# Kernel optimization log

Hardware: AMD Instinct MI355X
Metric: run time of the kernel (lower is better)

The kernel has to match this reference:

```python
import math
import jax, jax.numpy as jnp
import numpy as np

HIDDEN = 1024

def setup_inputs() -> dict:
    key = jax.random.key(0)
    kx, kq, kk, kv = jax.random.split(key, 4)
    scale = 1.0 / math.sqrt(HIDDEN)
    x = jax.random.normal(kx, (4, 2048, HIDDEN), dtype=jnp.float32)
    # nn.Linear weights, stored as [out, in] like torch; y = x @ W.T
    Wq = jax.random.normal(kq, (HIDDEN, HIDDEN), dtype=jnp.float32) * scale
    Wk = jax.random.normal(kk, (HIDDEN, HIDDEN), dtype=jnp.float32) * scale
    Wv = jax.random.normal(kv, (HIDDEN, HIDDEN), dtype=jnp.float32) * scale
    return {"x": x, "Wq": Wq, "Wk": Wk, "Wv": Wv}

def reference(x, Wq, Wk, Wv):
    # Q,K,V: [b, s, d]
    Q = jnp.einsum('bsd,ed->bse', x, Wq)
    K = jnp.einsum('bsd,ed->bse', x, Wk)
    V = jnp.einsum('bsd,ed->bse', x, Wv)
    scores = jnp.einsum('bqd,bkd->bqk', Q, K) / math.sqrt(x.shape[-1])
    att = jax.nn.softmax(scores, axis=-1)  # stable max-subtracted softmax, same math as _softmax
    return jnp.einsum('bqk,bkd->bqd', att, V)
```

## Files before the change

kernel.cpp:

```cpp
#include <hip/hip_runtime.h>
#include <stdint.h>

typedef unsigned int uint;
typedef unsigned short ushort;
typedef __attribute__((ext_vector_type(8))) short short8;
typedef __attribute__((ext_vector_type(16))) float floatx16;

#define MEG (1024u * 1024u)

__device__ inline ushort f2b(float f) {
  union { float f; uint u; } c; c.f = f;
  uint u = c.u;
  u = (u + 0x7fffu + ((u >> 16) & 1u)) >> 16;
  return (ushort)u;
}
__device__ inline float b2f(ushort u) {
  union { uint i; float f; } c; c.i = ((uint)u) << 16; return c.f;
}

__device__ inline void gl_lds16(const ushort* g, ushort* l) {
  __builtin_amdgcn_global_load_lds(
      (const __attribute__((address_space(1))) void*)g,
      (__attribute__((address_space(3))) void*)l, 16, 0, 0);
}

__global__ __launch_bounds__(256) void cvt_all(
    const float* __restrict__ x,  const float* __restrict__ wq,
    const float* __restrict__ wk, const float* __restrict__ wv,
    ushort* __restrict__ xb, ushort* __restrict__ wb)
{
  const int b = blockIdx.x;
  const float* s; ushort* d; int i;
  if (b < 4096) {
    s = x; d = xb; i = b * 256 + threadIdx.x;
  } else {
    int t = b - 4096;
    int wsel = t >> 9;
    s = (wsel == 0) ? wq : (wsel == 1) ? wk : wv;
    d = wb + (size_t)wsel * MEG;
    i = (t & 511) * 256 + threadIdx.x;
  }
  float4 a = ((const float4*)s)[i * 2];
  float4 c = ((const float4*)s)[i * 2 + 1];
  short8 v;
  v[0] = (short)f2b(a.x); v[1] = (short)f2b(a.y);
  v[2] = (short)f2b(a.z); v[3] = (short)f2b(a.w);
  v[4] = (short)f2b(c.x); v[5] = (short)f2b(c.y);
  v[6] = (short)f2b(c.z); v[7] = (short)f2b(c.w);
  ((short8*)d)[i] = v;
}

template <int MODE, int BN>
__device__ __forceinline__ void gemm_core(
    const ushort* __restrict__ A, int lda, size_t sA,
    const ushort* __restrict__ B, int ldb, size_t sB,
    void* __restrict__ C, int ldc, size_t sC,
    int K, float scale, float* __restrict__ Lsum)
{
  constexpr int NJ = BN / 64;
  constexpr int NB = BN / 32;
  __shared__ ushort As[128 * 64];
  __shared__ ushort Bs[BN * 64];
  __shared__ float Linv[(MODE == 2) ? 128 : 1];

  const int tid = threadIdx.x;
  const int bz  = blockIdx.z;
  A += (size_t)bz * sA;
  B += (size_t)bz * sB;

  const int m0 = blockIdx.y * 128;
  const int n0 = blockIdx.x * BN;

  const int lane = tid & 63;
  const int w    = tid >> 6;
  const int l32  = lane & 31;
  const int lh   = lane >> 5;
  const int mw   = w >> 1;
  const int nw   = w & 1;

  if constexpr (MODE == 2) {
    if (tid < 128) {
      float s = 0.f;
#pragma unroll
      for (int p = 0; p < 32; ++p)
        s += Lsum[((size_t)p * gridDim.z + bz) * 2048 + m0 + tid];
      Linv[tid] = 1.0f / s;
    }
  }

  const int srow = tid >> 3;
  const ushort* agp[4];
  const ushort* bgp[NB];
#pragma unroll
  for (int c4 = 0; c4 < 4; ++c4) {
    int r   = c4 * 32 + srow;
    int col = (((tid & 7) ^ ((r ^ (r >> 3)) & 7))) * 8;
    agp[c4] = A + (size_t)(m0 + r) * lda + col;
  }
#pragma unroll
  for (int cb = 0; cb < NB; ++cb) {
    int r   = cb * 32 + srow;
    int col = (((tid & 7) ^ ((r ^ (r >> 3)) & 7))) * 8;
    bgp[cb] = B + (size_t)(n0 + r) * ldb + col;
  }

  int arow[2], aswz[2], brow[NJ], bswz[NJ];
#pragma unroll
  for (int t = 0; t < 2; ++t) {
    arow[t] = mw * 64 + t * 32 + l32;
    aswz[t] = (arow[t] ^ (arow[t] >> 3)) & 7;
  }
#pragma unroll
  for (int t = 0; t < NJ; ++t) {
    brow[t] = nw * (BN / 2) + t * 32 + l32;
    bswz[t] = (brow[t] ^ (brow[t] >> 3)) & 7;
  }

  floatx16 acc[2][NJ];
#pragma unroll
  for (int i = 0; i < 2; ++i)
#pragma unroll
    for (int j = 0; j < NJ; ++j)
#pragma unroll
      for (int r = 0; r < 16; ++r) acc[i][j][r] = 0.f;

  for (int k0 = 0; k0 < K; k0 += 64) {
    __syncthreads();
#pragma unroll
    for (int c4 = 0; c4 < 4; ++c4) {
      gl_lds16(agp[c4], &As[(c4 * 32 + w * 8) * 64]);
      agp[c4] += 64;
    }
#pragma unroll
    for (int cb = 0; cb < NB; ++cb) {
      gl_lds16(bgp[cb], &Bs[(cb * 32 + w * 8) * 64]);
      bgp[cb] += 64;
    }
    __syncthreads();

#pragma unroll
    for (int s = 0; s < 4; ++s) {
      short8 af[2], bf[NJ];
#pragma unroll
      for (int t = 0; t < 2; ++t)
        af[t] = *(const short8*)&As[arow[t] * 64 + (((s * 2 + lh) ^ aswz[t]) * 8)];
#pragma unroll
      for (int t = 0; t < NJ; ++t)
        bf[t] = *(const short8*)&Bs[brow[t] * 64 + (((s * 2 + lh) ^ bswz[t]) * 8)];
#pragma unroll
      for (int i = 0; i < 2; ++i)
#pragma unroll
        for (int j = 0; j < NJ; ++j)
          acc[i][j] = __builtin_amdgcn_mfma_f32_32x32x16_bf16(
              af[i], bf[j], acc[i][j], 0, 0, 0);
    }
  }

  if constexpr (MODE == 0) {
#pragma unroll
    for (int i = 0; i < 2; ++i)
#pragma unroll
      for (int j = 0; j < NJ; ++j) {
        const int mbase = m0 + mw * 64 + i * 32 + 4 * lh;
        const int ng    = n0 + nw * (BN / 2) + j * 32 + l32;
        if (ng < 2048) {
          ushort* dst = (ushort*)C + (size_t)(ng >> 10) * (8u * MEG);
          const int nn = ng & 1023;
#pragma unroll
          for (int g = 0; g < 4; ++g)
#pragma unroll
            for (int r = 0; r < 4; ++r)
              dst[(size_t)(mbase + 8 * g + r) * 1024 + nn] =
                  f2b(acc[i][j][4 * g + r]);
        } else {
          ushort* Vo = (ushort*)C + (size_t)16 * MEG;
#pragma unroll
          for (int g = 0; g < 4; ++g) {
            uint lo = (uint)f2b(acc[i][j][4 * g + 0]) |
                      ((uint)f2b(acc[i][j][4 * g + 1]) << 16);
            uint hi = (uint)f2b(acc[i][j][4 * g + 2]) |
                      ((uint)f2b(acc[i][j][4 * g + 3]) << 16);
            *(uint2*)&Vo[(size_t)(ng - 2048) * 8192 + mbase + 8 * g] =
                make_uint2(lo, hi);
          }
        }
      }
  } else if constexpr (MODE == 1) {
    ushort* Cb = (ushort*)C + (size_t)bz * sC;
    float* Lp = Lsum + ((size_t)(blockIdx.x * 2 + nw) * gridDim.z + bz) * 2048;
    const int ng0 = n0 + nw * (BN / 2) + l32;
#pragma unroll
    for (int i = 0; i < 2; ++i) {
      const int mbase = m0 + mw * 64 + i * 32 + 4 * lh;
#pragma unroll
      for (int g = 0; g < 4; ++g)
#pragma unroll
        for (int r = 0; r < 4; ++r) {
          const int mg = mbase + 8 * g + r;
          float p0 = exp2f(acc[i][0][4 * g + r] * scale);
          float p1 = exp2f(acc[i][NJ - 1][4 * g + r] * scale);
          ushort u0 = f2b(p0), u1 = f2b(p1);
          Cb[(size_t)mg * ldc + ng0]      = u0;
          Cb[(size_t)mg * ldc + ng0 + 32] = u1;
          float ps = b2f(u0) + b2f(u1);
#pragma unroll
          for (int d = 1; d < 32; d <<= 1) ps += __shfl_xor(ps, d);
          if (l32 == 0) Lp[mg] = ps;
        }
    }
  } else {
    float* Cb = (float*)C + (size_t)bz * sC;
#pragma unroll
    for (int i = 0; i < 2; ++i) {
      const int mbase = m0 + mw * 64 + i * 32 + 4 * lh;
#pragma unroll
      for (int g = 0; g < 4; ++g)
#pragma unroll
        for (int r = 0; r < 4; ++r) {
          const int mg = mbase + 8 * g + r;
          const float inv = Linv[mg - m0];
#pragma unroll
          for (int j = 0; j < NJ; ++j) {
            const int ng = n0 + nw * (BN / 2) + j * 32 + l32;
            Cb[(size_t)mg * ldc + ng] = acc[i][j][4 * g + r] * inv;
          }
        }
    }
  }
}

__global__ __launch_bounds__(256, 4) void gemm_qkv(
    const ushort* __restrict__ A, int lda, size_t sA,
    const ushort* __restrict__ B, int ldb, size_t sB,
    void* __restrict__ C, int ldc, size_t sC, int K, float scale,
    float* __restrict__ Lsum) {
  gemm_core<0, 128>(A, lda, sA, B, ldb, sB, C, ldc, sC, K, scale, Lsum);
}
__global__ __launch_bounds__(256, 4) void gemm_s(
    const ushort* __restrict__ A, int lda, size_t sA,
    const ushort* __restrict__ B, int ldb, size_t sB,
    void* __restrict__ C, int ldc, size_t sC, int K, float scale,
    float* __restrict__ Lsum) {
  gemm_core<1, 128>(A, lda, sA, B, ldb, sB, C, ldc, sC, K, scale, Lsum);
}
__global__ __launch_bounds__(256, 4) void gemm_pv(
    const ushort* __restrict__ A, int lda, size_t sA,
    const ushort* __restrict__ B, int ldb, size_t sB,
    void* __restrict__ C, int ldc, size_t sC, int K, float scale,
    float* __restrict__ Lsum) {
  gemm_core<2, 128>(A, lda, sA, B, ldb, sB, C, ldc, sC, K, scale, Lsum);
}

extern "C" void kernel_launch(void* const* d_in, const int* in_sizes, int n_in,
                              void* d_out, int out_size, void* d_ws, size_t ws_size,
                              hipStream_t stream) {
  const float* x  = (const float*)d_in[0];
  const float* Wq = (const float*)d_in[1];
  const float* Wk = (const float*)d_in[2];
  const float* Wv = (const float*)d_in[3];
  float* outp = (float*)d_out;

  const float SCALE = 1.4426950408889634f / 32.0f;

  ushort* W0 = (ushort*)d_ws;
  ushort* Qb = W0;
  ushort* Kb = W0 + (size_t)8 * MEG;
  ushort* Vt = W0 + (size_t)16 * MEG;
  ushort* xb = W0 + (size_t)24 * MEG;
  ushort* Wb = W0 + (size_t)32 * MEG;
  ushort* Pb = W0 + (size_t)24 * MEG;

  const size_t NEED_FULL = ((size_t)40 * MEG) * 2 + (size_t)32 * 4 * 2048 * 4;
  const bool full = ws_size >= NEED_FULL;
  float* Lp = full ? (float*)(W0 + (size_t)40 * MEG)
                   : (float*)(W0 + (size_t)28 * MEG);

  cvt_all<<<5632, 256, 0, stream>>>(x, Wq, Wk, Wv, xb, Wb);

  gemm_qkv<<<dim3(24, 64, 1), 256, 0, stream>>>(
      xb, 1024, 0, Wb, 1024, 0, Qb, 1024, 0, 1024, 1.f, nullptr);

  if (full) {
    gemm_s<<<dim3(16, 16, 4), 256, 0, stream>>>(
        Qb, 1024, (size_t)2048 * 1024, Kb, 1024, (size_t)2048 * 1024,
        Pb, 2048, (size_t)2048 * 2048, 1024, SCALE, Lp);
    gemm_pv<<<dim3(8, 16, 4), 256, 0, stream>>>(
        Pb, 2048, (size_t)2048 * 2048, Vt, 8192, 2048,
        outp, 1024, (size_t)2048 * 1024, 2048, 1.f, Lp);
  } else {
    for (int b = 0; b < 4; ++b) {
      gemm_s<<<dim3(16, 16, 1), 256, 0, stream>>>(
          Qb + (size_t)b * 2048 * 1024, 1024, 0,
          Kb + (size_t)b * 2048 * 1024, 1024, 0,
          Pb, 2048, 0, 1024, SCALE, Lp);
      gemm_pv<<<dim3(8, 16, 1), 256, 0, stream>>>(
          Pb, 2048, 0, Vt + (size_t)b * 2048, 8192, 0,
          outp + (size_t)b * 2048 * 1024, 1024, 0, 2048, 1.f, Lp);
    }
  }
}
```

Measured before the change: 245.7 us.

## Double-buffer LDS tiles with K=32 stages to overlap loads and MFMA

Replaces the single-buffered K=64 LDS tile loop with a two-slot double buffer over K=32 slices. The next slice is issued with global_load_lds before the current slice's MFMAs run, and the swizzle changes to match the 32-wide rows. The aim is to hide global-load latency behind compute and remove one barrier per iteration. In exchange there are twice as many iterations, each with less MFMA work to hide latency behind, and a narrower swizzle that may bring LDS bank conflicts.

```diff
diff --git a/kernel.cpp b/kernel.cpp
--- a/kernel.cpp
+++ b/kernel.cpp
@@ -58,9 +58,11 @@
     int K, float scale, float* __restrict__ Lsum)
 {
   constexpr int NJ = BN / 64;
-  constexpr int NB = BN / 32;
-  __shared__ ushort As[128 * 64];
-  __shared__ ushort Bs[BN * 64];
+  constexpr int BI = BN / 64;
+  constexpr int ASLOT = 128 * 32;
+  constexpr int BSLOT = BN * 32;
+  __shared__ ushort As[2 * ASLOT];
+  __shared__ ushort Bs[2 * BSLOT];
   __shared__ float Linv[(MODE == 2) ? 128 : 1];
 
   const int tid = threadIdx.x;
@@ -88,32 +90,31 @@
     }
   }
 
-  const int srow = tid >> 3;
-  const ushort* agp[4];
-  const ushort* bgp[NB];
-#pragma unroll
-  for (int c4 = 0; c4 < 4; ++c4) {
-    int r   = c4 * 32 + srow;
-    int col = (((tid & 7) ^ ((r ^ (r >> 3)) & 7))) * 8;
-    agp[c4] = A + (size_t)(m0 + r) * lda + col;
-  }
-#pragma unroll
-  for (int cb = 0; cb < NB; ++cb) {
-    int r   = cb * 32 + srow;
-    int col = (((tid & 7) ^ ((r ^ (r >> 3)) & 7))) * 8;
-    bgp[cb] = B + (size_t)(n0 + r) * ldb + col;
+  const int srow = tid >> 2;
+  const int sch  = tid & 3;
+  const ushort* agp[2];
+  const ushort* bgp[BI];
+#pragma unroll
+  for (int q = 0; q < 2; ++q) {
+    int r = q * 64 + srow;
+    agp[q] = A + (size_t)(m0 + r) * lda + ((sch ^ ((r >> 1) & 3)) * 8);
+  }
+#pragma unroll
+  for (int q = 0; q < BI; ++q) {
+    int r = q * 64 + srow;
+    bgp[q] = B + (size_t)(n0 + r) * ldb + ((sch ^ ((r >> 1) & 3)) * 8);
   }
 
   int arow[2], aswz[2], brow[NJ], bswz[NJ];
 #pragma unroll
   for (int t = 0; t < 2; ++t) {
     arow[t] = mw * 64 + t * 32 + l32;
-    aswz[t] = (arow[t] ^ (arow[t] >> 3)) & 7;
+    aswz[t] = (arow[t] >> 1) & 3;
   }
 #pragma unroll
   for (int t = 0; t < NJ; ++t) {
     brow[t] = nw * (BN / 2) + t * 32 + l32;
-    bswz[t] = (brow[t] ^ (brow[t] >> 3)) & 7;
+    bswz[t] = (brow[t] >> 1) & 3;
   }
 
   floatx16 acc[2][NJ];
@@ -124,29 +125,38 @@
 #pragma unroll
       for (int r = 0; r < 16; ++r) acc[i][j][r] = 0.f;
 
-  for (int k0 = 0; k0 < K; k0 += 64) {
-    __syncthreads();
-#pragma unroll
-    for (int c4 = 0; c4 < 4; ++c4) {
-      gl_lds16(agp[c4], &As[(c4 * 32 + w * 8) * 64]);
-      agp[c4] += 64;
-    }
-#pragma unroll
-    for (int cb = 0; cb < NB; ++cb) {
-      gl_lds16(bgp[cb], &Bs[(cb * 32 + w * 8) * 64]);
-      bgp[cb] += 64;
-    }
-    __syncthreads();
-
-#pragma unroll
-    for (int s = 0; s < 4; ++s) {
+  const int nt = K / 32;
+
+#define STAGE(slot)                                                       \
+  {                                                                       \
+    ushort* Ad = &As[(slot) * ASLOT];                                     \
+    ushort* Bd = &Bs[(slot) * BSLOT];                                     \
+    _Pragma("unroll")                                                     \
+    for (int q = 0; q < 2; ++q) {                                         \
+      gl_lds16(agp[q], Ad + (q * 64 + w * 16) * 32); agp[q] += 32;        \
+    }                                                                     \
+    _Pragma("unroll")                                                     \
+    for (int q = 0; q < BI; ++q) {                                        \
+      gl_lds16(bgp[q], Bd + (q * 64 + w * 16) * 32); bgp[q] += 32;        \
+    }                                                                     \
+  }
+
+  STAGE(0);
+  __syncthreads();
+
+  for (int t = 0; t < nt; ++t) {
+    const ushort* At = &As[(t & 1) * ASLOT];
+    const ushort* Bt = &Bs[(t & 1) * BSLOT];
+    if (t + 1 < nt) STAGE((t + 1) & 1);
+#pragma unroll
+    for (int s = 0; s < 2; ++s) {
       short8 af[2], bf[NJ];
 #pragma unroll
-      for (int t = 0; t < 2; ++t)
-        af[t] = *(const short8*)&As[arow[t] * 64 + (((s * 2 + lh) ^ aswz[t]) * 8)];
-#pragma unroll
-      for (int t = 0; t < NJ; ++t)
-        bf[t] = *(const short8*)&Bs[brow[t] * 64 + (((s * 2 + lh) ^ bswz[t]) * 8)];
+      for (int i = 0; i < 2; ++i)
+        af[i] = *(const short8*)&At[arow[i] * 32 + (((s * 2 + lh) ^ aswz[i]) * 8)];
+#pragma unroll
+      for (int j = 0; j < NJ; ++j)
+        bf[j] = *(const short8*)&Bt[brow[j] * 32 + (((s * 2 + lh) ^ bswz[j]) * 8)];
 #pragma unroll
       for (int i = 0; i < 2; ++i)
 #pragma unroll
@@ -154,7 +164,9 @@
           acc[i][j] = __builtin_amdgcn_mfma_f32_32x32x16_bf16(
               af[i], bf[j], acc[i][j], 0, 0, 0);
     }
-  }
+    __syncthreads();
+  }
+#undef STAGE
 
   if constexpr (MODE == 0) {
 #pragma unroll
```

After: 268.8 us. 1.09x slower.

## Give PV GEMM a dedicated double-buffered LDS pipeline kernel

Applied to the files above, without the earlier changes.

Splits the P·V GEMM out of the shared templated core into its own kernel. The new kernel double-buffers the A and B tiles in LDS, issuing the global-to-LDS loads for the next K tile while MFMAs run on the current one, with one barrier per iteration. The aim is to hide global load latency in the long-K (2048) PV product. It doubles LDS usage, so launch bounds drop to 2 blocks per SM, which may lower occupancy.

```diff
diff --git a/kernel.cpp b/kernel.cpp
--- a/kernel.cpp
+++ b/kernel.cpp
@@ -61,7 +61,6 @@
   constexpr int NB = BN / 32;
   __shared__ ushort As[128 * 64];
   __shared__ ushort Bs[BN * 64];
-  __shared__ float Linv[(MODE == 2) ? 128 : 1];
 
   const int tid = threadIdx.x;
   const int bz  = blockIdx.z;
@@ -77,16 +76,6 @@
   const int lh   = lane >> 5;
   const int mw   = w >> 1;
   const int nw   = w & 1;
-
-  if constexpr (MODE == 2) {
-    if (tid < 128) {
-      float s = 0.f;
-#pragma unroll
-      for (int p = 0; p < 32; ++p)
-        s += Lsum[((size_t)p * gridDim.z + bz) * 2048 + m0 + tid];
-      Linv[tid] = 1.0f / s;
-    }
-  }
 
   const int srow = tid >> 3;
   const ushort* agp[4];
@@ -185,7 +174,7 @@
           }
         }
       }
-  } else if constexpr (MODE == 1) {
+  } else {
     ushort* Cb = (ushort*)C + (size_t)bz * sC;
     float* Lp = Lsum + ((size_t)(blockIdx.x * 2 + nw) * gridDim.z + bz) * 2048;
     const int ng0 = n0 + nw * (BN / 2) + l32;
@@ -208,24 +197,6 @@
           if (l32 == 0) Lp[mg] = ps;
         }
     }
-  } else {
-    float* Cb = (float*)C + (size_t)bz * sC;
-#pragma unroll
-    for (int i = 0; i < 2; ++i) {
-      const int mbase = m0 + mw * 64 + i * 32 + 4 * lh;
-#pragma unroll
-      for (int g = 0; g < 4; ++g)
-#pragma unroll
-        for (int r = 0; r < 4; ++r) {
-          const int mg = mbase + 8 * g + r;
-          const float inv = Linv[mg - m0];
-#pragma unroll
-          for (int j = 0; j < NJ; ++j) {
-            const int ng = n0 + nw * (BN / 2) + j * 32 + l32;
-            Cb[(size_t)mg * ldc + ng] = acc[i][j][4 * g + r] * inv;
-          }
-        }
-    }
   }
 }
 
@@ -243,12 +214,127 @@
     float* __restrict__ Lsum) {
   gemm_core<1, 128>(A, lda, sA, B, ldb, sB, C, ldc, sC, K, scale, Lsum);
 }
-__global__ __launch_bounds__(256, 4) void gemm_pv(
+
+__global__ __launch_bounds__(256, 2) void gemm_pv(
     const ushort* __restrict__ A, int lda, size_t sA,
     const ushort* __restrict__ B, int ldb, size_t sB,
     void* __restrict__ C, int ldc, size_t sC, int K, float scale,
-    float* __restrict__ Lsum) {
-  gemm_core<2, 128>(A, lda, sA, B, ldb, sB, C, ldc, sC, K, scale, Lsum);
+    float* __restrict__ Lsum)
+{
+  constexpr int SLOT = 128 * 64;
+  __shared__ ushort As[2 * SLOT];
+  __shared__ ushort Bs[2 * SLOT];
+  __shared__ float Linv[128];
+
+  const int tid = threadIdx.x;
+  const int bz  = blockIdx.z;
+  A += (size_t)bz * sA;
+  B += (size_t)bz * sB;
+
+  const int m0 = blockIdx.y * 128;
+  const int n0 = blockIdx.x * 128;
+
+  const int lane = tid & 63;
+  const int w    = tid >> 6;
+  const int l32  = lane & 31;
+  const int lh   = lane >> 5;
+  const int mw   = w >> 1;
+  const int nw   = w & 1;
+
+  if (tid < 128) {
+    float s = 0.f;
+#pragma unroll
+    for (int p = 0; p < 32; ++p)
+      s += Lsum[((size_t)p * gridDim.z + bz) * 2048 + m0 + tid];
+    Linv[tid] = 1.0f / s;
+  }
+
+  const int srow = tid >> 3;
+  const ushort* agp[4];
+  const ushort* bgp[4];
+#pragma unroll
+  for (int c4 = 0; c4 < 4; ++c4) {
+    int r   = c4 * 32 + srow;
+    int col = (((tid & 7) ^ ((r ^ (r >> 3)) & 7))) * 8;
+    agp[c4] = A + (size_t)(m0 + r) * lda + col;
+    bgp[c4] = B + (size_t)(n0 + r) * ldb + col;
+  }
+
+  int arow[2], aswz[2], brow[2], bswz[2];
+#pragma unroll
+  for (int t = 0; t < 2; ++t) {
+    arow[t] = mw * 64 + t * 32 + l32;
+    aswz[t] = (arow[t] ^ (arow[t] >> 3)) & 7;
+    brow[t] = nw * 64 + t * 32 + l32;
+    bswz[t] = (brow[t] ^ (brow[t] >> 3)) & 7;
+  }
+
+  floatx16 acc[2][2];
+#pragma unroll
+  for (int i = 0; i < 2; ++i)
+#pragma unroll
+    for (int j = 0; j < 2; ++j)
+#pragma unroll
+      for (int r = 0; r < 16; ++r) acc[i][j][r] = 0.f;
+
+  const int nt = K / 64;
+
+#define PV_STAGE(slot)                                                    \
+  {                                                                       \
+    ushort* Ad = &As[(slot) * SLOT];                                      \
+    ushort* Bd = &Bs[(slot) * SLOT];                                      \
+    _Pragma("unroll")                                                     \
+    for (int c4 = 0; c4 < 4; ++c4) {                                      \
+      gl_lds16(agp[c4], Ad + (c4 * 32 + w * 8) * 64); agp[c4] += 64;      \
+      gl_lds16(bgp[c4], Bd + (c4 * 32 + w * 8) * 64); bgp[c4] += 64;      \
+    }                                                                     \
+  }
+
+  PV_STAGE(0);
+  __syncthreads();
+
+  for (int t = 0; t < nt; ++t) {
+    const ushort* At = &As[(t & 1) * SLOT];
+    const ushort* Bt = &Bs[(t & 1) * SLOT];
+    if (t + 1 < nt) PV_STAGE((t + 1) & 1);
+
+#pragma unroll
+    for (int s = 0; s < 4; ++s) {
+      short8 af[2], bf[2];
+#pragma unroll
+      for (int i = 0; i < 2; ++i)
+        af[i] = *(const short8*)&At[arow[i] * 64 + (((s * 2 + lh) ^ aswz[i]) * 8)];
+#pragma unroll
+      for (int j = 0; j < 2; ++j)
+        bf[j] = *(const short8*)&Bt[brow[j] * 64 + (((s * 2 + lh) ^ bswz[j]) * 8)];
+#pragma unroll
+      for (int i = 0; i < 2; ++i)
+#pragma unroll
+        for (int j = 0; j < 2; ++j)
+          acc[i][j] = __builtin_amdgcn_mfma_f32_32x32x16_bf16(
+              af[i], bf[j], acc[i][j], 0, 0, 0);
+    }
+    __syncthreads();
+  }
+#undef PV_STAGE
+
+  float* Cb = (float*)C + (size_t)bz * sC;
+#pragma unroll
+  for (int i = 0; i < 2; ++i) {
+    const int mbase = m0 + mw * 64 + i * 32 + 4 * lh;
+#pragma unroll
+    for (int g = 0; g < 4; ++g)
+#pragma unroll
+      for (int r = 0; r < 4; ++r) {
+        const int mg = mbase + 8 * g + r;
+        const float inv = Linv[mg - m0];
+#pragma unroll
+        for (int j = 0; j < 2; ++j) {
+          const int ng = n0 + nw * 64 + j * 32 + l32;
+          Cb[(size_t)mg * ldc + ng] = acc[i][j][4 * g + r] * inv;
+        }
+      }
+  }
 }
 
 extern "C" void kernel_launch(void* const* d_in, const int* in_sizes, int n_in,
```

Result: slower. 252.8 us (+2.9%).

## Split-K the PV GEMM in two and normalize in a separate combine kernel

Applied to the files above, without the earlier changes.

The P·V GEMM is split along its reduction dimension into two halves, which doubles the grid so more blocks run per CU. One half writes its partial sums to the output buffer and the other to a scratch buffer placed over the no-longer-needed Q/K workspace. A new elementwise combine kernel adds the two partials, recomputes the softmax row sums from the stored partial sums, and applies the 1/sum normalization. The in-GEMM normalization is removed. In exchange, an extra launch and roughly three full fp32 output-sized memory passes are added.

```diff
diff --git a/kernel.cpp b/kernel.cpp
--- a/kernel.cpp
+++ b/kernel.cpp
@@ -61,12 +61,17 @@
   constexpr int NB = BN / 32;
   __shared__ ushort As[128 * 64];
   __shared__ ushort Bs[BN * 64];
-  __shared__ float Linv[(MODE == 2) ? 128 : 1];
 
   const int tid = threadIdx.x;
-  const int bz  = blockIdx.z;
+  const int zz  = blockIdx.z;
+  const int bz  = (MODE == 2) ? (zz >> 1) : zz;
   A += (size_t)bz * sA;
   B += (size_t)bz * sB;
+  if constexpr (MODE == 2) {
+    const int ks = zz & 1;
+    A += ks * 1024;
+    B += ks * 1024;
+  }
 
   const int m0 = blockIdx.y * 128;
   const int n0 = blockIdx.x * BN;
@@ -77,16 +82,6 @@
   const int lh   = lane >> 5;
   const int mw   = w >> 1;
   const int nw   = w & 1;
-
-  if constexpr (MODE == 2) {
-    if (tid < 128) {
-      float s = 0.f;
-#pragma unroll
-      for (int p = 0; p < 32; ++p)
-        s += Lsum[((size_t)p * gridDim.z + bz) * 2048 + m0 + tid];
-      Linv[tid] = 1.0f / s;
-    }
-  }
 
   const int srow = tid >> 3;
   const ushort* agp[4];
@@ -209,7 +204,7 @@
         }
     }
   } else {
-    float* Cb = (float*)C + (size_t)bz * sC;
+    float* Cb = ((zz & 1) ? (float*)C : Lsum) + (size_t)bz * sC;
 #pragma unroll
     for (int i = 0; i < 2; ++i) {
       const int mbase = m0 + mw * 64 + i * 32 + 4 * lh;
@@ -218,11 +213,10 @@
 #pragma unroll
         for (int r = 0; r < 4; ++r) {
           const int mg = mbase + 8 * g + r;
-          const float inv = Linv[mg - m0];
 #pragma unroll
           for (int j = 0; j < NJ; ++j) {
             const int ng = n0 + nw * (BN / 2) + j * 32 + l32;
-            Cb[(size_t)mg * ldc + ng] = acc[i][j][4 * g + r] * inv;
+            Cb[(size_t)mg * ldc + ng] = acc[i][j][4 * g + r];
           }
         }
     }
@@ -249,6 +243,29 @@
     void* __restrict__ C, int ldc, size_t sC, int K, float scale,
     float* __restrict__ Lsum) {
   gemm_core<2, 128>(A, lda, sA, B, ldb, sB, C, ldc, sC, K, scale, Lsum);
+}
+
+__global__ __launch_bounds__(256) void combine(
+    float* __restrict__ out, const float* __restrict__ o0,
+    const float* __restrict__ Lp, int nz)
+{
+  const size_t base = ((size_t)blockIdx.x * 256 + threadIdx.x) * 16;
+  const size_t rowg = base >> 10;
+  const int bz  = (int)(rowg >> 11);
+  const int row = (int)(rowg & 2047);
+  float s = 0.f;
+#pragma unroll
+  for (int p = 0; p < 32; ++p)
+    s += Lp[((size_t)p * nz + bz) * 2048 + row];
+  const float inv = 1.0f / s;
+  const float4* a = (const float4*)(o0 + base);
+  float4* b = (float4*)(out + base);
+#pragma unroll
+  for (int j = 0; j < 4; ++j) {
+    float4 x = b[j], y = a[j];
+    b[j] = make_float4((x.x + y.x) * inv, (x.y + y.y) * inv,
+                       (x.z + y.z) * inv, (x.w + y.w) * inv);
+  }
 }
 
 extern "C" void kernel_launch(void* const* d_in, const int* in_sizes, int n_in,
@@ -284,18 +301,22 @@
     gemm_s<<<dim3(16, 16, 4), 256, 0, stream>>>(
         Qb, 1024, (size_t)2048 * 1024, Kb, 1024, (size_t)2048 * 1024,
         Pb, 2048, (size_t)2048 * 2048, 1024, SCALE, Lp);
-    gemm_pv<<<dim3(8, 16, 4), 256, 0, stream>>>(
+    float* o0 = (float*)W0;
+    gemm_pv<<<dim3(8, 16, 8), 256, 0, stream>>>(
         Pb, 2048, (size_t)2048 * 2048, Vt, 8192, 2048,
-        outp, 1024, (size_t)2048 * 1024, 2048, 1.f, Lp);
+        outp, 1024, (size_t)2048 * 1024, 1024, 1.f, o0);
+    combine<<<2048, 256, 0, stream>>>(outp, o0, Lp, 4);
   } else {
+    float* o0 = (float*)(W0 + (size_t)30 * MEG);
     for (int b = 0; b < 4; ++b) {
       gemm_s<<<dim3(16, 16, 1), 256, 0, stream>>>(
           Qb + (size_t)b * 2048 * 1024, 1024, 0,
           Kb + (size_t)b * 2048 * 1024, 1024, 0,
           Pb, 2048, 0, 1024, SCALE, Lp);
-      gemm_pv<<<dim3(8, 16, 1), 256, 0, stream>>>(
+      gemm_pv<<<dim3(8, 16, 2), 256, 0, stream>>>(
           Pb, 2048, 0, Vt + (size_t)b * 2048, 8192, 0,
-          outp + (size_t)b * 2048 * 1024, 1024, 0, 2048, 1.f, Lp);
-    }
-  }
-}
+          outp + (size_t)b * 2048 * 1024, 1024, 0, 1024, 1.f, o0);
+      combine<<<512, 256, 0, stream>>>(outp + (size_t)b * 2048 * 1024, o0, Lp, 1);
+    }
+  }
+}
```

Measured after the change: 275.9 us. +12.3%, slower.
